# Optimization experiments

Hardware: AMD Instinct MI355X
Metric: run time of the kernel (lower is better)

The kernel has to match this reference:

```python
import jax, jax.numpy as jnp
import numpy as np

NUM_CLASSES = 80
C_OUT = 81
SCORE_THR = 0.02
IOU_THR = 0.45
TOPK = 1000
IMG_MAX = 320.0
STRIDES = [16, 32, 64, 107, 160, 320]
MIN_SIZES = [48, 100, 150, 202, 253, 304]
MAX_SIZES = [100, 150, 202, 253, 304, 320]
FEAT = [20, 10, 5, 3, 2, 1]
MAX_RATIO = float(abs(np.log(0.016)))


def _base_anchors(level):
    base = float(MIN_SIZES[level])
    scales = np.array([1.0, np.sqrt(MAX_SIZES[level] / MIN_SIZES[level])])
    ratios = np.array([1.0, 0.5, 2.0, 1.0 / 3.0, 3.0])
    h_ratios = np.sqrt(ratios)
    w_ratios = 1.0 / h_ratios
    # scale_major=False: scales vary along rows
    ws = (base * scales[:, None] * w_ratios[None, :]).reshape(-1)
    hs = (base * scales[:, None] * h_ratios[None, :]).reshape(-1)
    c = STRIDES[level] / 2.0
    ba = np.stack([c - 0.5 * ws, c - 0.5 * hs, c + 0.5 * ws, c + 0.5 * hs], -1)
    return ba[[0, 5, 1, 2, 3, 4]]  # index_select reorder, 6 anchors/loc


def _priors(level):
    ba = _base_anchors(level)
    f, s = FEAT[level], STRIDES[level]
    sx = np.arange(f, dtype=np.float64) * s
    xx = np.tile(sx, f)
    yy = np.repeat(sx, f)
    shifts = np.stack([xx, yy, xx, yy], -1)  # [f*f,4]
    return (ba[None, :, :] + shifts[:, None, :]).reshape(-1, 4).astype(np.float32)


PRIORS = [jnp.asarray(_priors(i)) for i in range(6)]


def delta2bbox(priors, deltas):
    stds = jnp.array([0.1, 0.1, 0.2, 0.2], dtype=deltas.dtype)
    d = deltas * stds
    pxy = (priors[:, :2] + priors[:, 2:]) * 0.5
    pwh = priors[:, 2:] - priors[:, :2]
    dwh = jnp.clip(d[:, 2:], -MAX_RATIO, MAX_RATIO)
    gxy = pxy + pwh * d[:, :2]
    gwh = pwh * jnp.exp(dwh)
    boxes = jnp.concatenate([gxy - 0.5 * gwh, gxy + 0.5 * gwh], -1)
    return jnp.clip(boxes, 0.0, IMG_MAX)


def _nms_keep(boxes, valid, iou_thr):
    # greedy NMS over score-sorted boxes; returns bool keep mask
    K = boxes.shape[0]
    area = (boxes[:, 2] - boxes[:, 0]) * (boxes[:, 3] - boxes[:, 1])
    lt = jnp.maximum(boxes[:, None, :2], boxes[None, :, :2])
    rb = jnp.minimum(boxes[:, None, 2:], boxes[None, :, 2:])
    wh = jnp.clip(rb - lt, 0.0)
    inter = wh[..., 0] * wh[..., 1]
    iou = inter / (area[:, None] + area[None, :] - inter)
    ar = jnp.arange(K)

    def body(i, alive):
        sup = (iou[i] > iou_thr) & (ar > i) & alive[i]
        return alive & ~sup

    return jax.lax.fori_loop(0, K, body, valid)


def _single_image(cls_list, bb_list):
    boxes_l, scores_l, labels_l, valid_l = [], [], [], []
    for cls, bb, priors in zip(cls_list, bb_list, PRIORS):
        probs = jax.nn.softmax(cls.transpose(1, 2, 0).reshape(-1, C_OUT), axis=-1)[:, :NUM_CLASSES]
        flat = probs.reshape(-1)  # [N*80]
        k = min(TOPK, flat.shape[0])
        masked = jnp.where(flat > SCORE_THR, flat, -1.0)
        vals, idx = jax.lax.top_k(masked, k)
        valid = vals > SCORE_THR
        a_idx = idx // NUM_CLASSES
        lbl = idx % NUM_CLASSES
        deltas = bb.transpose(1, 2, 0).reshape(-1, 4)[a_idx]
        boxes = delta2bbox(priors[a_idx], deltas)
        boxes_l.append(boxes)
        scores_l.append(jnp.where(valid, vals, 0.0))
        labels_l.append(lbl)
        valid_l.append(valid)
    boxes = jnp.concatenate(boxes_l, 0)   # [K,4]
    scores = jnp.concatenate(scores_l, 0)
    labels = jnp.concatenate(labels_l, 0)
    valid = jnp.concatenate(valid_l, 0)

    # batched (class-aware) NMS via per-class coordinate offsets
    max_coord = boxes.max()
    offsets = labels.astype(boxes.dtype) * (max_coord + 1.0)
    boxes_nms = boxes + offsets[:, None]
    order = jnp.argsort(-jnp.where(valid, scores, -jnp.inf))
    boxes_s = boxes[order]
    scores_s = scores[order]
    labels_s = labels[order]
    valid_s = valid[order]
    keep = jax.lax.stop_gradient(
        _nms_keep(jax.lax.stop_gradient(boxes_nms[order]), valid_s, IOU_THR))
    dets = jnp.concatenate([boxes_s, scores_s[:, None]], -1) * keep[:, None].astype(boxes.dtype)
    return dets, labels_s, keep


def setup_inputs() -> dict:
    key = jax.random.key(0)
    ks = jax.random.split(key, 12)
    B = 4
    inp = {}
    for i, f in enumerate(FEAT):
        inp[f"cls{i}"] = jax.random.normal(ks[i], (B, 486, f, f), dtype=jnp.float32)
        inp[f"bb{i}"] = jax.random.normal(ks[6 + i], (B, 24, f, f), dtype=jnp.float32)
    return inp


def reference(cls0, cls1, cls2, cls3, cls4, cls5, bb0, bb1, bb2, bb3, bb4, bb5):
    def one(c0, c1, c2, c3, c4, c5, b0, b1, b2, b3, b4, b5):
        return _single_image([c0, c1, c2, c3, c4, c5], [b0, b1, b2, b3, b4, b5])
    dets, labels, keep = jax.vmap(one)(cls0, cls1, cls2, cls3, cls4, cls5,
                                       bb0, bb1, bb2, bb3, bb4, bb5)
    return dets, labels, keep
```

## Files before the change

### kernel.cpp

```cpp
#include <hip/hip_runtime.h>
#include <stdint.h>

#define NB 4
#define KTOT 5480
#define PER_IMG 258720
#define SCORE_THR 0.02f
#define IOU_THR 0.45f
#define REL_BASE 0x3CA3D70Bu
#define JCH 10
#define JSZ 548
#define ICH 11
#define NMSCAP 512
#define HBINS 512

__constant__ int cFEAT[6]    = {20,10,5,3,2,1};
__constant__ int cSTRIDE[6]  = {16,32,64,107,160,320};
__constant__ int cMIN[6]     = {48,100,150,202,253,304};
__constant__ int cMAX[6]     = {100,150,202,253,304,320};
__constant__ int cNFLAT[6]   = {192000,48000,12000,4320,1920,480};
__constant__ int cFLATOFF[6] = {0,192000,240000,252000,256320,258240};
__constant__ int cKSEL[6]    = {1000,1000,1000,1000,1000,480};
__constant__ int cKOFF[6]    = {0,1000,2000,3000,4000,5000};
__constant__ double cRATIO[6] = {1.0,1.0,0.5,2.0,1.0/3.0,3.0};
__constant__ int eTLEV[14]   = {0,0,0,0,0,0,0,0,1,1,2,3,4,5};
__constant__ int eTCHK[14]   = {0,1,2,3,4,5,6,7,0,1,0,0,0,0};
__constant__ int eNCH[6]     = {8,2,1,1,1,1};
__constant__ int hL0[6]      = {0,42,54,60,66,72};
__constant__ int hLN[6]      = {42,12,6,6,6,6};

__device__ __forceinline__ unsigned long long mk_key(unsigned kb, int lev, unsigned idx) {
  return ((unsigned long long)kb << 21) |
         (unsigned long long)(0x1FFFFFu ^ (((unsigned)lev << 18) | idx));
}

__device__ __forceinline__ unsigned long long shfl64(unsigned long long x, int src) {
  int lo = __shfl((int)(unsigned)(x & 0xffffffffull), src);
  int hi = __shfl((int)(unsigned)(x >> 32), src);
  return ((unsigned long long)(unsigned)hi << 32) | (unsigned)lo;
}

__global__ __launch_bounds__(256) void k_softmax(
    const float* __restrict__ c0, const float* __restrict__ c1,
    const float* __restrict__ c2, const float* __restrict__ c3,
    const float* __restrict__ c4, const float* __restrict__ c5,
    float* __restrict__ scores, unsigned* __restrict__ bhist,
    unsigned* __restrict__ obmax_u, unsigned* __restrict__ ctrl)
{
  int t = blockIdx.x;
  int tid = threadIdx.x;
  if (t == 0) {
    if (tid < 4) obmax_u[tid] = 0u;
    if (tid >= 64 && tid < 256) ctrl[tid - 64] = 0u;
  }
  int b = t / 78, rem = t % 78;
  int lev, a, cb;
  if (rem < 42)      { lev = 0; a = rem / 7;         cb = (rem % 7) * 64; }
  else if (rem < 54) { lev = 1; a = (rem - 42) >> 1; cb = ((rem - 42) & 1) * 64; }
  else               { lev = 2 + (rem - 54) / 6; a = (rem - 54) % 6; cb = 0; }
  const float* cls = (lev==0)?c0:(lev==1)?c1:(lev==2)?c2:(lev==3)?c3:(lev==4)?c4:c5;
  int f = cFEAT[lev], ff = f * f;
  int ncell = ff - cb; if (ncell > 64) ncell = 64;

  __shared__ float tile[81 * 64];
  __shared__ unsigned hcnt[HBINS];
  for (int i = tid; i < HBINS; i += 256) hcnt[i] = 0;
  const float* base = cls + (size_t)(b * 486 + a * 81) * ff + cb;
  for (int t2 = tid; t2 < 81 * 64; t2 += 256) {
    int c = t2 >> 6, cell = t2 & 63;
    if (cell < ncell)
      tile[(c << 6) | (cell ^ (c & 63))] = base[c * ff + cell];
  }
  __syncthreads();

  int lane = tid & 63, w = tid >> 6;
  for (int cell = w; cell < ncell; cell += 4) {
    float v1 = tile[(lane << 6) | (cell ^ lane)];
    float v2 = (lane <= 16) ? tile[((lane + 64) << 6) | (cell ^ lane)]
                            : __uint_as_float(0xff800000u);
    float mx = fmaxf(v1, v2);
    #pragma unroll
    for (int m = 32; m; m >>= 1) mx = fmaxf(mx, __shfl_xor(mx, m));
    float e1 = expf(v1 - mx);
    float e2 = (lane <= 16) ? expf(v2 - mx) : 0.f;
    float sm = e1 + e2;
    #pragma unroll
    for (int m = 32; m; m >>= 1) sm += __shfl_xor(sm, m);
    int row = (cb + cell) * 6 + a;
    float* out = scores + (size_t)b * PER_IMG + cFLATOFF[lev] + row * 80;
    float p1 = e1 / sm;
    out[lane] = (p1 > SCORE_THR) ? p1 : -1.f;
    if (p1 > SCORE_THR)
      atomicAdd(&hcnt[(__float_as_uint(p1) - REL_BASE) >> 17], 1u);
    if (lane < 16) {
      float p2 = e2 / sm;
      out[lane + 64] = (p2 > SCORE_THR) ? p2 : -1.f;
      if (p2 > SCORE_THR)
        atomicAdd(&hcnt[(__float_as_uint(p2) - REL_BASE) >> 17], 1u);
    }
  }
  __syncthreads();
  unsigned* hb = bhist + (size_t)t * HBINS;
  for (int i = tid; i < HBINS; i += 256) hb[i] = hcnt[i];
}

__global__ __launch_bounds__(256) void k_emit(
    const float* __restrict__ scores, const unsigned* __restrict__ bhist,
    unsigned* __restrict__ ctrl, unsigned long long* __restrict__ selkeys,
    unsigned long long* __restrict__ eqg)
{
  int b = blockIdx.x / 14, ent = blockIdx.x % 14;
  int lev = eTLEV[ent], chk = eTCHK[ent];
  int task = b * 6 + lev;
  int n = cNFLAT[lev];
  int tid = threadIdx.x;
  const float* s = scores + (size_t)b * PER_IMG + cFLATOFF[lev];
  unsigned long long* out = selkeys + (size_t)b * KTOT + cKOFF[lev];

  if (lev == 5) {
    for (int i = tid; i < n; i += 256) {
      float v = s[i];
      unsigned kb = (v > SCORE_THR) ? __float_as_uint(v) : 0u;
      out[i] = mk_key(kb, lev, (unsigned)i);
    }
    return;
  }

  unsigned k = (unsigned)cKSEL[lev];
  __shared__ unsigned long long wbuf[1024];
  __shared__ unsigned long long ebuf[4096];
  __shared__ unsigned sc[256];
  __shared__ unsigned wcnt, ecnt, sbw, sbe, sh_mode, sh_b1;

  {
    unsigned h0 = 0, h1 = 0;
    int hbase = b * 78 + hL0[lev];
    for (int j = 0; j < hLN[lev]; ++j) {
      const unsigned* hb = bhist + (size_t)(hbase + j) * HBINS;
      h0 += hb[2 * tid];
      h1 += hb[2 * tid + 1];
    }
    sc[tid] = h0 + h1;
    __syncthreads();
    for (int off = 1; off < 256; off <<= 1) {
      unsigned cur = sc[tid];
      unsigned add = (tid + off < 256) ? sc[tid + off] : 0u;
      __syncthreads();
      sc[tid] = cur + add;
      __syncthreads();
    }
    unsigned c = sc[0];
    if (tid == 0 && c < k) sh_mode = 1u;
    if (c >= k) {
      unsigned above = (tid == 255) ? 0u : sc[tid + 1];
      unsigned run = above;
      if (run < k && run + h1 >= k) { sh_mode = 0u; sh_b1 = (unsigned)(2 * tid + 1); }
      run += h1;
      if (run < k && run + h0 >= k) { sh_mode = 0u; sh_b1 = (unsigned)(2 * tid); }
    }
    if (tid == 0) { wcnt = 0; ecnt = 0; }
    __syncthreads();
  }
  unsigned mode = sh_mode;

  int csz = n / eNCH[lev];
  int start = chk * csz;
  const float4* s4 = (const float4*)(s + start);
  int n4 = csz >> 2;

  if (mode == 0u) {
    unsigned b1 = sh_b1;
    unsigned base_lo = REL_BASE + (b1 << 17);
    unsigned base_hi = base_lo + (1u << 17);
    #pragma unroll 4
    for (int i0 = tid; i0 < n4; i0 += 256) {
      float4 vv = s4[i0];
      #pragma unroll
      for (int e2 = 0; e2 < 4; ++e2) {
        float v = (e2==0)?vv.x:(e2==1)?vv.y:(e2==2)?vv.z:vv.w;
        if (v > SCORE_THR) {
          unsigned kb = __float_as_uint(v);
          unsigned idx = (unsigned)(start + i0 * 4 + e2);
          if (kb >= base_hi) {
            unsigned p = atomicAdd(&wcnt, 1u);
            if (p < 1024u) wbuf[p] = mk_key(kb, lev, idx);
          } else if (kb >= base_lo) {
            unsigned p = atomicAdd(&ecnt, 1u);
            if (p < 4096u) ebuf[p] = mk_key(kb, lev, idx);
          }
        }
      }
    }
  } else {
    #pragma unroll 4
    for (int i0 = tid; i0 < n4; i0 += 256) {
      float4 vv = s4[i0];
      #pragma unroll
      for (int e2 = 0; e2 < 4; ++e2) {
        float v = (e2==0)?vv.x:(e2==1)?vv.y:(e2==2)?vv.z:vv.w;
        if (v > SCORE_THR) {
          unsigned p = atomicAdd(&wcnt, 1u);
          if (p < 1024u) wbuf[p] = mk_key(__float_as_uint(v), lev,
                                          (unsigned)(start + i0 * 4 + e2));
        }
      }
    }
  }
  __syncthreads();
  if (tid == 0) {
    sbw = atomicAdd(&ctrl[task * 8 + 2], wcnt);
    sbe = atomicAdd(&ctrl[task * 8 + 3], ecnt);
  }
  __syncthreads();
  unsigned nw = (wcnt < 1024u) ? wcnt : 1024u;
  unsigned ne = (ecnt < 4096u) ? ecnt : 4096u;
  unsigned bw = sbw, be = sbe;
  for (unsigned t = tid; t < nw; t += 256) out[bw + t] = wbuf[t];
  for (unsigned t = tid; t < ne; t += 256) {
    unsigned g = be + t;
    if (g < 4096u) eqg[(size_t)task * 4096 + g] = ebuf[t];
  }
}

__global__ __launch_bounds__(1024) void k_finalize(
    const float* __restrict__ scores, const unsigned* __restrict__ bhist,
    const unsigned* __restrict__ ctrl, unsigned long long* __restrict__ selkeys,
    const unsigned long long* __restrict__ eqg)
{
  int task = blockIdx.x;
  int b = task / 6, lev = task % 6;
  if (lev == 5) return;
  int tid = threadIdx.x;
  unsigned k = (unsigned)cKSEL[lev];
  int n = cNFLAT[lev];
  const float* s = scores + (size_t)b * PER_IMG + cFLATOFF[lev];
  unsigned long long* out = selkeys + (size_t)b * KTOT + cKOFF[lev];
  unsigned levtag = (unsigned)lev << 18;

  __shared__ unsigned long long eqb[4096];
  __shared__ unsigned sc[1024];
  __shared__ unsigned sh_cnt, sh_eq, sh_byte, sh_r;

  unsigned hval = 0;
  if (tid < HBINS) {
    int hbase = b * 78 + hL0[lev];
    for (int j = 0; j < hLN[lev]; ++j)
      hval += bhist[(size_t)(hbase + j) * HBINS + tid];
  }
  sc[tid] = (tid < HBINS) ? hval : 0u;
  __syncthreads();
  for (int off = 1; off < 1024; off <<= 1) {
    unsigned cur = sc[tid];
    unsigned add = (tid + off < 1024) ? sc[tid + off] : 0u;
    __syncthreads();
    sc[tid] = cur + add;
    __syncthreads();
  }
  unsigned c = sc[0];
  __syncthreads();
  unsigned mode = (c >= k) ? 0u : 1u;
  bool done = false;

  if (mode == 0u) {
    unsigned cnt = ctrl[task * 8 + 2];
    unsigned e = ctrl[task * 8 + 3];
    unsigned need = k - cnt;
    if (e <= 4096u) {
      const unsigned long long* eq = eqg + (size_t)task * 4096;
      if (e == need) {
        for (unsigned t = tid; t < need; t += 1024) out[cnt + t] = eq[t];
      } else {
        unsigned P = 1; while (P < e) P <<= 1;
        for (unsigned t = tid; t < P; t += 1024) eqb[t] = (t < e) ? eq[t] : 0ull;
        __syncthreads();
        for (unsigned sz = 2; sz <= P; sz <<= 1)
          for (unsigned st = sz >> 1; st; st >>= 1) {
            for (unsigned w = tid; w < P / 2; w += 1024) {
              unsigned i = ((w & ~(st - 1)) << 1) | (w & (st - 1));
              unsigned l = i | st;
              bool up = ((i & sz) == 0);
              unsigned long long A = eqb[i], B = eqb[l];
              if ((A < B) == up) { eqb[i] = B; eqb[l] = A; }
            }
            __syncthreads();
          }
        for (unsigned t = tid; t < need; t += 1024) out[cnt + t] = eqb[t];
      }
      done = true;
    }
  } else {
    unsigned c2 = ctrl[task * 8 + 2];
    unsigned need = k - c2;
    unsigned base = 0;
    for (int start = 0; start < n && base < need; start += 1024) {
      int i = start + tid;
      unsigned pred = (i < n && !(s[i] > SCORE_THR)) ? 1u : 0u;
      sc[tid] = pred;
      __syncthreads();
      for (int off = 1; off < 1024; off <<= 1) {
        unsigned add = (tid >= off) ? sc[tid - off] : 0u;
        unsigned v = sc[tid];
        __syncthreads();
        sc[tid] = v + add;
        __syncthreads();
      }
      unsigned incl = sc[tid];
      unsigned total = sc[1023];
      unsigned excl = incl - pred;
      if (pred && (base + excl) < need)
        out[c2 + base + excl] =
            (unsigned long long)(0x1FFFFFu ^ (levtag | (unsigned)i));
      __syncthreads();
      base += total;
    }
    done = true;
  }

  if (!done) {
    unsigned* hist = sc;
    unsigned* equ = (unsigned*)eqb;
    unsigned prefix = 0, r = k;
    for (int pass = 3; pass >= 0; --pass) {
      int shift = pass * 8;
      for (int i = tid; i < 256; i += 1024) hist[i] = 0;
      __syncthreads();
      for (int i = tid; i < n; i += 1024) {
        float v = s[i];
        unsigned kb = (v > SCORE_THR) ? __float_as_uint(v) : 0u;
        bool match = (pass == 3) || (((kb ^ prefix) >> (shift + 8)) == 0u);
        if (match) atomicAdd(&hist[(kb >> shift) & 255u], 1u);
      }
      __syncthreads();
      if (tid == 0) {
        unsigned cum = 0, byte = 0, rr = r;
        for (int bb = 255; bb >= 0; --bb) {
          unsigned hh = hist[bb];
          if (cum + hh >= r) { byte = (unsigned)bb; rr = r - cum; break; }
          cum += hh;
        }
        sh_byte = byte; sh_r = rr;
      }
      __syncthreads();
      prefix |= (sh_byte << shift);
      r = sh_r;
      __syncthreads();
    }
    unsigned Kstar = prefix;
    if (tid == 0) { sh_cnt = 0; sh_eq = 0; }
    __syncthreads();
    for (int i = tid; i < n; i += 1024) {
      float v = s[i];
      unsigned kb = (v > SCORE_THR) ? __float_as_uint(v) : 0u;
      if (kb > Kstar) {
        unsigned slot = atomicAdd(&sh_cnt, 1u);
        out[slot] = mk_key(kb, lev, (unsigned)i);
      } else if (kb == Kstar) {
        unsigned es = atomicAdd(&sh_eq, 1u);
        if (es < 4096u) equ[es] = (unsigned)i;
      }
    }
    __syncthreads();
    unsigned m = sh_cnt;
    unsigned e2 = (sh_eq < 4096u) ? sh_eq : 4096u;
    unsigned need2 = k - m;
    if (e2 > need2) {
      unsigned P = 1; while (P < e2) P <<= 1;
      for (unsigned t = tid; t < P; t += 1024) if (t >= e2) equ[t] = 0xFFFFFFFFu;
      __syncthreads();
      for (unsigned sz = 2; sz <= P; sz <<= 1)
        for (unsigned st = sz >> 1; st; st >>= 1) {
          for (unsigned w = tid; w < P / 2; w += 1024) {
            unsigned i = ((w & ~(st - 1)) << 1) | (w & (st - 1));
            unsigned l = i | st;
            bool up = ((i & sz) == 0);
            unsigned A = equ[i], B = equ[l];
            if ((A > B) == up) { equ[i] = B; equ[l] = A; }
          }
          __syncthreads();
        }
    }
    __syncthreads();
    for (unsigned t = tid; t < need2; t += 1024)
      out[m + t] = ((unsigned long long)Kstar << 21) |
                   (unsigned long long)(0x1FFFFFu ^ (levtag | equ[t]));
  }
}

__global__ __launch_bounds__(512) void k_rank(
    const unsigned long long* __restrict__ selkeys, unsigned* __restrict__ rank_part)
{
  int blk = blockIdx.x;
  int jc = blk % JCH;
  int rest = blk / JCH;
  int ic = rest % ICH, b = rest / ICH;
  int tid = threadIdx.x;
  __shared__ __align__(16) unsigned long long sk[JSZ];
  const unsigned long long* keys = selkeys + (size_t)b * KTOT;
  for (int j = tid; j < JSZ; j += 512) sk[j] = keys[jc * JSZ + j];
  int i = ic * 512 + tid;
  unsigned long long mk = (i < KTOT) ? keys[i] : 0ull;
  __syncthreads();
  unsigned r = 0;
  const ulonglong2* sk2 = (const ulonglong2*)sk;
  #pragma unroll 8
  for (int j = 0; j < JSZ / 2; ++j) {
    ulonglong2 kk = sk2[j];
    r += (kk.x > mk) ? 1u : 0u;
    r += (kk.y > mk) ? 1u : 0u;
  }
  if (i < KTOT) rank_part[((size_t)jc * NB + b) * KTOT + i] = r;
}

__global__ __launch_bounds__(512) void k_decode(
    const unsigned long long* __restrict__ selkeys, const unsigned* __restrict__ rank_part,
    const float* __restrict__ g0, const float* __restrict__ g1,
    const float* __restrict__ g2, const float* __restrict__ g3,
    const float* __restrict__ g4, const float* __restrict__ g5,
    float* __restrict__ boxes, float* __restrict__ oscore,
    unsigned char* __restrict__ lab8, unsigned* __restrict__ obmax_u,
    float* __restrict__ outp)
{
  int b = blockIdx.x / ICH, ic = blockIdx.x % ICH;
  int tid = threadIdx.x;
  int i = ic * 512 + tid;
  __shared__ double ba[6][6][4];
  if (tid < 36) {
    int lev = tid / 6, a = tid % 6;
    double base = (double)cMIN[lev];
    double scl = (a == 1) ? sqrt((double)cMAX[lev] / (double)cMIN[lev]) : 1.0;
    double hr = sqrt(cRATIO[a]);
    double wr = 1.0 / hr;
    double wsz = base * scl * wr;
    double hsz = base * scl * hr;
    double cc = (double)cSTRIDE[lev] / 2.0;
    ba[lev][a][0] = cc - 0.5 * wsz;
    ba[lev][a][1] = cc - 0.5 * hsz;
    ba[lev][a][2] = cc + 0.5 * wsz;
    ba[lev][a][3] = cc + 0.5 * hsz;
  }
  __syncthreads();

  float lmax = 0.f;
  if (i < KTOT) {
    unsigned long long mk = selkeys[(size_t)b * KTOT + i];
    unsigned r = 0;
    #pragma unroll
    for (int jc = 0; jc < JCH; ++jc)
      r += rank_part[((size_t)jc * NB + b) * KTOT + i];
    unsigned tag = 0x1FFFFFu ^ (unsigned)(mk & 0x1FFFFFull);
    int lev = tag >> 18;
    int fi = tag & 0x3FFFF;
    unsigned vb2 = (unsigned)(mk >> 21);
    int valid = (vb2 != 0u);
    float score = valid ? __uint_as_float(vb2) : 0.f;
    int label = fi % 80;
    int arow = fi / 80;
    int a = arow % 6, cell = arow / 6;
    int f = cFEAT[lev], ff = f * f;
    int x = cell % f, y = cell / f;
    const float* gb = (lev==0)?g0:(lev==1)?g1:(lev==2)?g2:(lev==3)?g3:(lev==4)?g4:g5;
    const float* pb = gb + (size_t)(b * 24 + a * 4) * ff + y * f + x;
    float d0 = pb[0] * 0.1f, d1 = pb[ff] * 0.1f;
    float d2 = pb[2 * ff] * 0.2f, d3 = pb[3 * ff] * 0.2f;
    const float MR = (float)4.135166556742356;
    d2 = fminf(fmaxf(d2, -MR), MR);
    d3 = fminf(fmaxf(d3, -MR), MR);
    double shx = (double)(x * cSTRIDE[lev]);
    double shy = (double)(y * cSTRIDE[lev]);
    float p0 = (float)(ba[lev][a][0] + shx);
    float p1 = (float)(ba[lev][a][1] + shy);
    float p2 = (float)(ba[lev][a][2] + shx);
    float p3 = (float)(ba[lev][a][3] + shy);
    float pxc = (p0 + p2) * 0.5f, pyc = (p1 + p3) * 0.5f;
    float pw = p2 - p0, ph = p3 - p1;
    float gx = pxc + pw * d0, gy = pyc + ph * d1;
    float gw = pw * expf(d2), gh = ph * expf(d3);
    float x1 = gx - 0.5f * gw, y1 = gy - 0.5f * gh;
    float x2 = gx + 0.5f * gw, y2 = gy + 0.5f * gh;
    x1 = fminf(fmaxf(x1, 0.f), 320.f);
    y1 = fminf(fmaxf(y1, 0.f), 320.f);
    x2 = fminf(fmaxf(x2, 0.f), 320.f);
    y2 = fminf(fmaxf(y2, 0.f), 320.f);
    size_t o = (size_t)b * KTOT + (size_t)r;
    boxes[o * 4 + 0] = x1; boxes[o * 4 + 1] = y1;
    boxes[o * 4 + 2] = x2; boxes[o * 4 + 3] = y2;
    oscore[o] = score;
    lab8[o] = valid ? (unsigned char)label : (unsigned char)0xFF;
    outp[(size_t)NB * KTOT * 5 + o] = (float)label;
    if (!valid) {
      float* det = outp + o * 5;
      det[0] = 0.f; det[1] = 0.f; det[2] = 0.f; det[3] = 0.f; det[4] = 0.f;
      outp[(size_t)NB * KTOT * 6 + o] = 0.f;
    }
    lmax = fmaxf(fmaxf(x1, y1), fmaxf(x2, y2));
  }
  #pragma unroll
  for (int m = 32; m; m >>= 1) lmax = fmaxf(lmax, __shfl_xor(lmax, m));
  if ((tid & 63) == 0) atomicMax(&obmax_u[b], __float_as_uint(lmax));
}

__global__ __launch_bounds__(256) void k_nms(
    const float* __restrict__ boxes, const float* __restrict__ oscore,
    const unsigned char* __restrict__ lab8, const unsigned* __restrict__ obmax_u,
    float* __restrict__ out)
{
  int blk = blockIdx.x;
  int b = blk / 80, cls = blk % 80;
  int tid = threadIdx.x;
  int lane = tid & 63, w = tid >> 6;

  __shared__ unsigned short list[NMSCAP];
  __shared__ float ox1[NMSCAP], oy1[NMSCAP], ox2[NMSCAP], oy2[NMSCAP];
  __shared__ float oar[NMSCAP], osc[NMSCAP];
  __shared__ float rx1[NMSCAP], ry1[NMSCAP], rx2[NMSCAP], ry2[NMSCAP];
  __shared__ unsigned long long mask[NMSCAP][8];
  __shared__ unsigned ccnt[24], cbase[24];
  __shared__ int sh_n;
  __shared__ unsigned long long alive_s[8];

  float ofs = (float)cls * (__uint_as_float(obmax_u[b]) + 1.0f);
  const unsigned* lb32 = (const unsigned*)(lab8 + (size_t)b * KTOT);

  unsigned long long balA[6][4];
  #pragma unroll
  for (int ci = 0; ci < 6; ++ci) {
    int chunk = w + ci * 4;
    unsigned v = 0xFFFFFFFFu;
    if (chunk < 22) {
      int u = chunk * 64 + lane;
      if (u < KTOT / 4) v = lb32[u];
    }
    unsigned long long m0 = __ballot(((v      ) & 0xFFu) == (unsigned)cls);
    unsigned long long m1 = __ballot(((v >>  8) & 0xFFu) == (unsigned)cls);
    unsigned long long m2 = __ballot(((v >> 16) & 0xFFu) == (unsigned)cls);
    unsigned long long m3 = __ballot(((v >> 24) & 0xFFu) == (unsigned)cls);
    balA[ci][0] = m0; balA[ci][1] = m1; balA[ci][2] = m2; balA[ci][3] = m3;
    if (chunk < 22 && lane == 0)
      ccnt[chunk] = (unsigned)(__popcll(m0) + __popcll(m1) + __popcll(m2) + __popcll(m3));
  }
  __syncthreads();
  if (tid == 0) {
    unsigned tot = 0;
    for (int c = 0; c < 22; ++c) { cbase[c] = tot; tot += ccnt[c]; }
    sh_n = (tot < NMSCAP) ? (int)tot : NMSCAP;
  }
  __syncthreads();
  int n = sh_n;
  unsigned long long blt = (lane == 0) ? 0ull : ((~0ull) >> (64 - lane));
  #pragma unroll
  for (int ci = 0; ci < 6; ++ci) {
    int chunk = w + ci * 4;
    if (chunk < 22) {
      unsigned pos = cbase[chunk];
      unsigned below = (unsigned)(__popcll(balA[ci][0] & blt) + __popcll(balA[ci][1] & blt) +
                                  __popcll(balA[ci][2] & blt) + __popcll(balA[ci][3] & blt));
      unsigned within = 0;
      #pragma unroll
      for (int k = 0; k < 4; ++k) {
        if ((balA[ci][k] >> lane) & 1ull) {
          unsigned mypos = pos + below + within;
          if (mypos < NMSCAP) list[mypos] = (unsigned short)(chunk * 256 + lane * 4 + k);
          ++within;
        }
      }
    }
  }
  __syncthreads();

  for (int t = tid; t < n; t += 256) {
    int pos = list[t];
    size_t o = (size_t)b * KTOT + pos;
    float4 bb = *(const float4*)(boxes + o * 4);
    rx1[t] = bb.x; ry1[t] = bb.y; rx2[t] = bb.z; ry2[t] = bb.w;
    float a1 = bb.x + ofs, b1 = bb.y + ofs, a2 = bb.z + ofs, b2 = bb.w + ofs;
    ox1[t] = a1; oy1[t] = b1; ox2[t] = a2; oy2[t] = b2;
    oar[t] = (a2 - a1) * (b2 - b1);
    osc[t] = oscore[o];
  }
  __syncthreads();

  int nw = (n + 63) >> 6;
  for (int i = tid; i < n; i += 256) {
    float ax1 = ox1[i], ay1 = oy1[i], ax2 = ox2[i], ay2 = oy2[i], aar = oar[i];
    int w0 = i >> 6;
    for (int wd = w0; wd < nw; ++wd) {
      unsigned long long m = 0;
      int jbase = wd << 6;
      int jend = n - jbase; if (jend > 64) jend = 64;
      for (int jj = 0; jj < jend; ++jj) {
        int j = jbase + jj;
        if (j > i) {
          float ix1 = fmaxf(ax1, ox1[j]);
          float iy1 = fmaxf(ay1, oy1[j]);
          float ix2 = fminf(ax2, ox2[j]);
          float iy2 = fminf(ay2, oy2[j]);
          float iw = fmaxf(ix2 - ix1, 0.f);
          float ih = fmaxf(iy2 - iy1, 0.f);
          float inter = iw * ih;
          float iou = inter / (aar + oar[j] - inter);
          if (iou > IOU_THR) m |= (1ull << jj);
        }
      }
      mask[i][wd] = m;
    }
  }
  __syncthreads();

  if (w == 0) {
    unsigned long long aw = 0;
    if (lane < nw) {
      int rem = n - (lane << 6);
      aw = (rem >= 64) ? ~0ull : ((1ull << rem) - 1ull);
    }
    for (int i = 0; i < n; ++i) {
      int wi = i >> 6;
      unsigned long long mrow = (lane >= wi && lane < nw) ? mask[i][lane] : 0ull;
      unsigned long long tw = shfl64(aw, wi);
      if ((tw >> (i & 63)) & 1ull) aw &= ~mrow;
    }
    if (lane < 8) alive_s[lane] = aw;
  }
  __syncthreads();

  for (int t = tid; t < n; t += 256) {
    float kf = ((alive_s[t >> 6] >> (t & 63)) & 1ull) ? 1.f : 0.f;
    int pos = list[t];
    size_t o = (size_t)b * KTOT + pos;
    float* det = out + o * 5;
    det[0] = rx1[t] * kf; det[1] = ry1[t] * kf;
    det[2] = rx2[t] * kf; det[3] = ry2[t] * kf;
    det[4] = osc[t] * kf;
    out[(size_t)NB * KTOT * 6 + o] = kf;
  }
}

extern "C" void kernel_launch(void* const* d_in, const int* in_sizes, int n_in,
                              void* d_out, int out_size, void* d_ws, size_t ws_size,
                              hipStream_t stream) {
  (void)in_sizes; (void)n_in; (void)out_size; (void)ws_size;
  const float* cls[6]; const float* bbx[6];
  for (int i = 0; i < 6; ++i) {
    cls[i] = (const float*)d_in[2 * i];
    bbx[i] = (const float*)d_in[2 * i + 1];
  }
  char* ws = (char*)d_ws;
  float* scores = (float*)ws;
  unsigned* rank_part = (unsigned*)ws;
  unsigned long long* selkeys = (unsigned long long*)(ws + 4139520);
  float* boxes  = (float*)(ws + 4314880);
  float* oscore = (float*)(ws + 4665600);
  unsigned char* lab8 = (unsigned char*)(ws + 4753280);
  unsigned* obmax_u = (unsigned*)(ws + 5016320);
  unsigned* ctrl    = (unsigned*)(ws + 5016576);
  unsigned* bhist   = (unsigned*)(ws + 5017600);
  unsigned long long* eqg = (unsigned long long*)(ws + 5656576);

  k_softmax<<<NB * 78, 256, 0, stream>>>(cls[0], cls[1], cls[2], cls[3], cls[4], cls[5],
                                         scores, bhist, obmax_u, ctrl);
  k_emit<<<NB * 14, 256, 0, stream>>>(scores, bhist, ctrl, selkeys, eqg);
  k_finalize<<<24, 1024, 0, stream>>>(scores, bhist, ctrl, selkeys, eqg);
  k_rank<<<NB * ICH * JCH, 512, 0, stream>>>(selkeys, rank_part);
  k_decode<<<NB * ICH, 512, 0, stream>>>(selkeys, rank_part, bbx[0], bbx[1], bbx[2],
                                         bbx[3], bbx[4], bbx[5], boxes, oscore, lab8,
                                         obmax_u, (float*)d_out);
  k_nms<<<NB * 80, 256, 0, stream>>>(boxes, oscore, lab8, obmax_u, (float*)d_out);
}
```

Before: 105.4 us.

## Halve histogram bins, transpose partial-histogram layout, and split emit into more chunks

```diff
diff --git a/kernel.cpp b/kernel.cpp
--- a/kernel.cpp
+++ b/kernel.cpp
@@ -11,7 +11,8 @@
 #define JSZ 548
 #define ICH 11
 #define NMSCAP 512
-#define HBINS 512
+#define HBINS 256
+#define HPART 42
 
 __constant__ int cFEAT[6]    = {20,10,5,3,2,1};
 __constant__ int cSTRIDE[6]  = {16,32,64,107,160,320};
@@ -22,11 +23,11 @@
 __constant__ int cKSEL[6]    = {1000,1000,1000,1000,1000,480};
 __constant__ int cKOFF[6]    = {0,1000,2000,3000,4000,5000};
 __constant__ double cRATIO[6] = {1.0,1.0,0.5,2.0,1.0/3.0,3.0};
-__constant__ int eTLEV[14]   = {0,0,0,0,0,0,0,0,1,1,2,3,4,5};
-__constant__ int eTCHK[14]   = {0,1,2,3,4,5,6,7,0,1,0,0,0,0};
-__constant__ int eNCH[6]     = {8,2,1,1,1,1};
-__constant__ int hL0[6]      = {0,42,54,60,66,72};
-__constant__ int hLN[6]      = {42,12,6,6,6,6};
+__constant__ int eTLEV[24] = {0,0,0,0,0,0,0,0,0,0,0,0,0,0,0,0, 1,1,1,1, 2,3,4,5};
+__constant__ int eTCHK[24] = {0,1,2,3,4,5,6,7,8,9,10,11,12,13,14,15, 0,1,2,3, 0,0,0,0};
+__constant__ int eNCH[6]   = {16,4,1,1,1,1};
+__constant__ int hL0[6]    = {0,42,54,60,66,72};
+__constant__ int hLN[6]    = {42,12,6,6,6,6};
 
 __device__ __forceinline__ unsigned long long mk_key(unsigned kb, int lev, unsigned idx) {
   return ((unsigned long long)kb << 21) |
@@ -63,7 +64,7 @@
 
   __shared__ float tile[81 * 64];
   __shared__ unsigned hcnt[HBINS];
-  for (int i = tid; i < HBINS; i += 256) hcnt[i] = 0;
+  if (tid < HBINS) hcnt[tid] = 0;
   const float* base = cls + (size_t)(b * 486 + a * 81) * ff + cb;
   for (int t2 = tid; t2 < 81 * 64; t2 += 256) {
     int c = t2 >> 6, cell = t2 & 63;
@@ -90,17 +91,19 @@
     float p1 = e1 / sm;
     out[lane] = (p1 > SCORE_THR) ? p1 : -1.f;
     if (p1 > SCORE_THR)
-      atomicAdd(&hcnt[(__float_as_uint(p1) - REL_BASE) >> 17], 1u);
+      atomicAdd(&hcnt[(__float_as_uint(p1) - REL_BASE) >> 18], 1u);
     if (lane < 16) {
       float p2 = e2 / sm;
       out[lane + 64] = (p2 > SCORE_THR) ? p2 : -1.f;
       if (p2 > SCORE_THR)
-        atomicAdd(&hcnt[(__float_as_uint(p2) - REL_BASE) >> 17], 1u);
-    }
-  }
-  __syncthreads();
-  unsigned* hb = bhist + (size_t)t * HBINS;
-  for (int i = tid; i < HBINS; i += 256) hb[i] = hcnt[i];
+        atomicAdd(&hcnt[(__float_as_uint(p2) - REL_BASE) >> 18], 1u);
+    }
+  }
+  __syncthreads();
+  int task = b * 6 + lev;
+  int j = rem - hL0[lev];
+  if (tid < HBINS)
+    bhist[((size_t)task * HBINS + tid) * HPART + j] = hcnt[tid];
 }
 
 __global__ __launch_bounds__(256) void k_emit(
@@ -108,7 +111,7 @@
     unsigned* __restrict__ ctrl, unsigned long long* __restrict__ selkeys,
     unsigned long long* __restrict__ eqg)
 {
-  int b = blockIdx.x / 14, ent = blockIdx.x % 14;
+  int b = blockIdx.x / 24, ent = blockIdx.x % 24;
   int lev = eTLEV[ent], chk = eTCHK[ent];
   int task = b * 6 + lev;
   int n = cNFLAT[lev];
@@ -132,14 +135,11 @@
   __shared__ unsigned wcnt, ecnt, sbw, sbe, sh_mode, sh_b1;
 
   {
-    unsigned h0 = 0, h1 = 0;
-    int hbase = b * 78 + hL0[lev];
-    for (int j = 0; j < hLN[lev]; ++j) {
-      const unsigned* hb = bhist + (size_t)(hbase + j) * HBINS;
-      h0 += hb[2 * tid];
-      h1 += hb[2 * tid + 1];
-    }
-    sc[tid] = h0 + h1;
+    const unsigned* hb = bhist + ((size_t)task * HBINS + tid) * HPART;
+    int np = hLN[lev];
+    unsigned cnt = 0;
+    for (int j = 0; j < np; ++j) cnt += hb[j];
+    sc[tid] = cnt;
     __syncthreads();
     for (int off = 1; off < 256; off <<= 1) {
       unsigned cur = sc[tid];
@@ -152,10 +152,7 @@
     if (tid == 0 && c < k) sh_mode = 1u;
     if (c >= k) {
       unsigned above = (tid == 255) ? 0u : sc[tid + 1];
-      unsigned run = above;
-      if (run < k && run + h1 >= k) { sh_mode = 0u; sh_b1 = (unsigned)(2 * tid + 1); }
-      run += h1;
-      if (run < k && run + h0 >= k) { sh_mode = 0u; sh_b1 = (unsigned)(2 * tid); }
+      if (above < k && above + cnt >= k) { sh_mode = 0u; sh_b1 = (unsigned)tid; }
     }
     if (tid == 0) { wcnt = 0; ecnt = 0; }
     __syncthreads();
@@ -169,8 +166,8 @@
 
   if (mode == 0u) {
     unsigned b1 = sh_b1;
-    unsigned base_lo = REL_BASE + (b1 << 17);
-    unsigned base_hi = base_lo + (1u << 17);
+    unsigned base_lo = REL_BASE + (b1 << 18);
+    unsigned base_hi = base_lo + (1u << 18);
     #pragma unroll 4
     for (int i0 = tid; i0 < n4; i0 += 256) {
       float4 vv = s4[i0];
@@ -242,17 +239,14 @@
 
   unsigned hval = 0;
   if (tid < HBINS) {
-    int hbase = b * 78 + hL0[lev];
-    for (int j = 0; j < hLN[lev]; ++j)
-      hval += bhist[(size_t)(hbase + j) * HBINS + tid];
+    const unsigned* hb = bhist + ((size_t)task * HBINS + tid) * HPART;
+    int np = hLN[lev];
+    for (int j = 0; j < np; ++j) hval += hb[j];
   }
   sc[tid] = (tid < HBINS) ? hval : 0u;
   __syncthreads();
-  for (int off = 1; off < 1024; off <<= 1) {
-    unsigned cur = sc[tid];
-    unsigned add = (tid + off < 1024) ? sc[tid + off] : 0u;
-    __syncthreads();
-    sc[tid] = cur + add;
+  for (int off = 128; off >= 1; off >>= 1) {
+    if (tid < off) sc[tid] += sc[tid + off];
     __syncthreads();
   }
   unsigned c = sc[0];
@@ -652,11 +646,11 @@
   unsigned* obmax_u = (unsigned*)(ws + 5016320);
   unsigned* ctrl    = (unsigned*)(ws + 5016576);
   unsigned* bhist   = (unsigned*)(ws + 5017600);
-  unsigned long long* eqg = (unsigned long long*)(ws + 5656576);
+  unsigned long long* eqg = (unsigned long long*)(ws + 6049792);
 
   k_softmax<<<NB * 78, 256, 0, stream>>>(cls[0], cls[1], cls[2], cls[3], cls[4], cls[5],
                                          scores, bhist, obmax_u, ctrl);
-  k_emit<<<NB * 14, 256, 0, stream>>>(scores, bhist, ctrl, selkeys, eqg);
+  k_emit<<<NB * 24, 256, 0, stream>>>(scores, bhist, ctrl, selkeys, eqg);
   k_finalize<<<24, 1024, 0, stream>>>(scores, bhist, ctrl, selkeys, eqg);
   k_rank<<<NB * ICH * JCH, 512, 0, stream>>>(selkeys, rank_part);
   k_decode<<<NB * ICH, 512, 0, stream>>>(selkeys, rank_part, bbx[0], bbx[1], bbx[2],
```

Result: faster. 96.12 us, median of 2 (-8.8%).
